# Optimization experiments

Measured on AMD Instinct MI355X. Metric: run time of the kernel, lower is better.

Reference implementation:

```python
import jax, jax.numpy as jnp
import numpy as np
from jax import lax

THRESH = 0.1  # stand-in for os.environ['THRESHOLD']
DN = ('NCHW', 'OIHW', 'NCHW')


def _prelu(x, a):
    # nn.PReLU() with a single shared parameter a (init 0.25)
    return jnp.where(x >= 0, x, a[0] * x)


def _nan_conv(x, w, b):
    # NaNConv2d: skip (zero out) input activations with |x| < THRESH,
    # then a standard 3x3 conv, stride 1, padding 1.
    xm = jnp.where(jnp.abs(x) >= THRESH, x, jnp.zeros((), x.dtype))
    y = lax.conv_general_dilated(xm, w, window_strides=(1, 1),
                                 padding='SAME', dimension_numbers=DN)
    return y + b[None, :, None, None]


def setup_inputs() -> dict:
    key = jax.random.key(0)
    ks = jax.random.split(key, 8)
    B, C, H, W = 8, 256, 128, 128
    x = jax.random.normal(ks[0], (B, C, H, W), dtype=jnp.float32)
    w_scale = 0.05  # keep activations numerically tame
    w1 = jax.random.normal(ks[1], (C, C, 3, 3), dtype=jnp.float32) * w_scale
    b1 = jax.random.normal(ks[2], (C,), dtype=jnp.float32) * w_scale
    w2 = jax.random.normal(ks[3], (C, C, 3, 3), dtype=jnp.float32) * w_scale
    b2 = jax.random.normal(ks[4], (C,), dtype=jnp.float32) * w_scale
    w3 = jax.random.normal(ks[5], (C, C, 3, 3), dtype=jnp.float32) * w_scale
    b3 = jax.random.normal(ks[6], (C,), dtype=jnp.float32) * w_scale
    prelu_a = jnp.full((1,), 0.25, dtype=jnp.float32)  # nn.PReLU default init
    return {'x': x, 'w1': w1, 'b1': b1, 'w2': w2, 'b2': b2,
            'w3': w3, 'b3': b3, 'prelu_a': prelu_a}


def reference(x, w1, b1, w2, b2, w3, b3, prelu_a):
    # x0 = NaNConv(prelu(x))
    x0 = _nan_conv(_prelu(x, prelu_a), w1, b1)
    # cat+max over trailing dim == elementwise max
    x1_max = jnp.maximum(x, x0)
    x1 = _prelu(x1_max, prelu_a)
    x1c = _nan_conv(x1, w2, b2)
    x2_max = jnp.maximum(x1c, x1_max)
    x2 = _prelu(x2_max, prelu_a)
    out = _nan_conv(x2, w3, b3)
    return out
```

## Files before the change

kernel.cpp:

```cpp
#include <hip/hip_runtime.h>
#include <cstddef>

#define THRESH 0.1f

constexpr int Bn = 8, C = 256, H = 128, W = 128;
constexpr int HW = H * W;
constexpr size_t CHW = (size_t)C * HW;
constexpr int WSZ = 9 * 256 * 256;

typedef __attribute__((ext_vector_type(8))) short short8;
typedef __attribute__((ext_vector_type(4))) float f32x4;

__device__ __forceinline__ float bf2f(ushort u) {
    union { unsigned u; float f; } v; v.u = ((unsigned)u) << 16; return v.f;
}
__device__ __forceinline__ ushort f2bf(float f) {
    union { float f; unsigned u; } v; v.f = f;
    unsigned r = v.u + 0x7FFF + ((v.u >> 16) & 1);
    return (ushort)(r >> 16);
}
__device__ __forceinline__ float pm(float x, float a) {
    float t = (x >= 0.f) ? x : a * x;
    return (fabsf(t) >= THRESH) ? t : 0.f;
}

__device__ __forceinline__ void load_lds16(const void* g, void* l) {
    __builtin_amdgcn_global_load_lds(
        (const __attribute__((address_space(1))) unsigned int*)g,
        (__attribute__((address_space(3))) unsigned int*)l, 16, 0, 0);
}

__global__ void wtrans_kernel(const float* __restrict__ w1,
                              const float* __restrict__ w2,
                              const float* __restrict__ w3,
                              ushort* __restrict__ Wtf)
{
    const float* src = (blockIdx.z == 0) ? w1 : (blockIdx.z == 1) ? w2 : w3;
    ushort* dst = Wtf + (size_t)blockIdx.z * WSZ;
    int idx = blockIdx.x * 256 + threadIdx.x;
    int co = idx >> 8, ci = idx & 255;
    int cb  = co >> 6;
    int m   = (co >> 4) & 3;
    int l15 = co & 15;
    int cib = ci >> 5;
    int l4  = (ci >> 3) & 3;
    int j   = ci & 7;
    int lane = l15 + 16 * l4;
    for (int t = 0; t < 9; ++t) {
        float v = src[((size_t)co * 256 + ci) * 9 + t];
        size_t o = ((((size_t)cb * 8 + cib) * 9 + t) * 4 + m) * 512 + lane * 8 + j;
        dst[o] = f2bf(v);
    }
}

__global__ __launch_bounds__(256) void xt1_kernel(const float* __restrict__ x,
                                                  const float* __restrict__ pa,
                                                  ushort* __restrict__ Xt)
{
    __shared__ float sl[64][133];
    int tid = threadIdx.x;
    int ci0 = blockIdx.x * 64, h = blockIdx.y, b = blockIdx.z;
    float a = pa[0];
    int wcol = tid & 127, chalf = tid >> 7;
    const float* xb = x + (size_t)b * CHW + (size_t)ci0 * HW + h * W;
    for (int r = 0; r < 32; ++r) {
        int ci = r * 2 + chalf;
        sl[ci][wcol] = pm(xb[(size_t)ci * HW + wcol], a);
    }
    __syncthreads();
    ushort* dst = Xt + ((size_t)(b * H + h)) * W * C + ci0;
    for (int r = 0; r < 4; ++r) {
        int c = r * 256 + tid;
        int wc = c >> 3, cic = c & 7;
        unsigned p0 = f2bf(sl[cic*8+0][wc]) | ((unsigned)f2bf(sl[cic*8+1][wc]) << 16);
        unsigned p1 = f2bf(sl[cic*8+2][wc]) | ((unsigned)f2bf(sl[cic*8+3][wc]) << 16);
        unsigned p2 = f2bf(sl[cic*8+4][wc]) | ((unsigned)f2bf(sl[cic*8+5][wc]) << 16);
        unsigned p3 = f2bf(sl[cic*8+6][wc]) | ((unsigned)f2bf(sl[cic*8+7][wc]) << 16);
        uint4 v = {p0, p1, p2, p3};
        *(uint4*)(dst + (size_t)wc * C + cic * 8) = v;
    }
}

template <int MODE>
__global__ __launch_bounds__(256, 2) void conv_kernel(
    const ushort* __restrict__ Xt, const ushort* __restrict__ Wtf,
    const float* __restrict__ bias, const float* __restrict__ pa,
    const float* __restrict__ xf,
    ushort* __restrict__ xmax,
    ushort* __restrict__ XtOut,
    float* __restrict__ out)
{
    __shared__ __align__(16) ushort sa[4 * 132 * 32];

    const int tid = threadIdx.x, lane = tid & 63, wv = tid >> 6;
    const int orig = blockIdx.x;
    const int vid = (orig & 7) * 256 + (orig >> 3);
    const int cb = vid & 3, by = vid >> 2;
    const int co0 = cb * 64;
    const int b = by >> 6, h0 = (by & 63) * 2;
    const int l15 = lane & 15, l4 = lane >> 4;
    const int hrow = wv >> 1, whalf = wv & 1;

    {
        uint4 z = {0, 0, 0, 0};
        uint4* zp = (uint4*)sa;
        for (int i = tid; i < 2112; i += 256) zp[i] = z;
    }

    f32x4 acc[4][4];
    const f32x4 z4 = {0.f, 0.f, 0.f, 0.f};
#pragma unroll
    for (int m = 0; m < 4; ++m)
#pragma unroll
        for (int n = 0; n < 4; ++n) acc[m][n] = z4;

    const ushort* xb = Xt + (size_t)b * H * W * C;
    const int sr = wv;
    const int shh = h0 - 1 + sr;
    const bool svalid = (unsigned)shh < 128u;
    const ushort* sgbase = xb + (size_t)shh * W * C;
    ushort* slbase = sa + (sr * 132 + 1) * 32;
    const int lchunk = lane >> 2, lsub = lane & 3;

    for (int cib = 0; cib < 8; ++cib) {
        const int ci0 = cib * 32;
        __syncthreads();
        if (svalid) {
#pragma unroll
            for (int seg = 0; seg < 8; ++seg) {
                int ww = seg * 16 + lchunk;
                int key = ((sr * 132 + 1 + ww) >> 1) & 3;
                const void* gp = sgbase + (size_t)ww * C + ci0 + ((lsub ^ key) << 3);
                load_lds16(gp, slbase + seg * 512);
            }
        }
        __syncthreads();

        const ushort* wB = Wtf + ((size_t)cb * 8 + cib) * 18432;
#pragma unroll
        for (int ky = 0; ky < 3; ++ky) {
            const int r = hrow + ky;
#pragma unroll
            for (int kx = 0; kx < 3; ++kx) {
                const int t = ky * 3 + kx;
                short8 af[4], bfv[4];
#pragma unroll
                for (int m = 0; m < 4; ++m)
                    af[m] = *(const short8*)(wB + (size_t)(t * 4 + m) * 512 + lane * 8);
#pragma unroll
                for (int n = 0; n < 4; ++n) {
                    int wi = whalf * 64 + n * 16 + l15 + kx;
                    int row = r * 132 + wi;
                    int key = (row >> 1) & 3;
                    bfv[n] = *(const short8*)(sa + row * 32 + ((l4 ^ key) << 3));
                }
#pragma unroll
                for (int m = 0; m < 4; ++m)
#pragma unroll
                    for (int n = 0; n < 4; ++n)
                        acc[m][n] = __builtin_amdgcn_mfma_f32_16x16x32_bf16(
                            af[m], bfv[n], acc[m][n], 0, 0, 0);
            }
        }
    }

    const int h = h0 + hrow;
    const float ap = (MODE != 0) ? pa[0] : 0.f;
#pragma unroll
    for (int m = 0; m < 4; ++m) {
        const int cobase = co0 + m * 16 + l4 * 4;
        const f32x4 bv = *(const f32x4*)(bias + cobase);
#pragma unroll
        for (int n = 0; n < 4; ++n) {
            const int wc = whalf * 64 + n * 16 + l15;
            if constexpr (MODE == 0) {
#pragma unroll
                for (int rr = 0; rr < 4; ++rr)
                    out[((size_t)(b * C + cobase + rr) * H + h) * W + wc] =
                        acc[m][n][rr] + bv[rr];
            } else {
                const size_t nb = ((size_t)(b * H + h) * W + wc) * C + cobase;
                float mm[4];
                if constexpr (MODE == 1) {
#pragma unroll
                    for (int rr = 0; rr < 4; ++rr) {
                        float vv = acc[m][n][rr] + bv[rr];
                        float xv = xf[((size_t)(b * C + cobase + rr) * H + h) * W + wc];
                        mm[rr] = fmaxf(xv, vv);
                    }
                    uint2 um = {(unsigned)f2bf(mm[0]) | ((unsigned)f2bf(mm[1]) << 16),
                                (unsigned)f2bf(mm[2]) | ((unsigned)f2bf(mm[3]) << 16)};
                    *(uint2*)(xmax + nb) = um;
                } else {
                    uint2 mv = *(const uint2*)(xmax + nb);
                    mm[0] = fmaxf(acc[m][n][0] + bv[0], bf2f((ushort)(mv.x & 0xffffu)));
                    mm[1] = fmaxf(acc[m][n][1] + bv[1], bf2f((ushort)(mv.x >> 16)));
                    mm[2] = fmaxf(acc[m][n][2] + bv[2], bf2f((ushort)(mv.y & 0xffffu)));
                    mm[3] = fmaxf(acc[m][n][3] + bv[3], bf2f((ushort)(mv.y >> 16)));
                }
                uint2 px = {(unsigned)f2bf(pm(mm[0], ap)) | ((unsigned)f2bf(pm(mm[1], ap)) << 16),
                            (unsigned)f2bf(pm(mm[2], ap)) | ((unsigned)f2bf(pm(mm[3], ap)) << 16)};
                *(uint2*)(XtOut + nb) = px;
            }
        }
    }
}

extern "C" void kernel_launch(void* const* d_in, const int* in_sizes, int n_in,
                              void* d_out, int out_size, void* d_ws, size_t ws_size,
                              hipStream_t stream)
{
    const float* x  = (const float*)d_in[0];
    const float* w1 = (const float*)d_in[1];
    const float* b1 = (const float*)d_in[2];
    const float* w2 = (const float*)d_in[3];
    const float* b2 = (const float*)d_in[4];
    const float* w3 = (const float*)d_in[5];
    const float* b3 = (const float*)d_in[6];
    const float* pa = (const float*)d_in[7];

    char* ws = (char*)d_ws;
    ushort* Xt1  = (ushort*)ws;
    ushort* Xt2  = (ushort*)(ws + 67108864);
    ushort* xmax = (ushort*)(ws + 134217728);
    ushort* Wtf  = (ushort*)(ws + 201326592);

    dim3 tg(4, 128, 8), tb(256);

    wtrans_kernel<<<dim3(256, 1, 3), 256, 0, stream>>>(w1, w2, w3, Wtf);
    xt1_kernel<<<tg, tb, 0, stream>>>(x, pa, Xt1);
    conv_kernel<1><<<dim3(2048), tb, 0, stream>>>(Xt1, Wtf, b1, pa, x, xmax, Xt2, nullptr);
    conv_kernel<2><<<dim3(2048), tb, 0, stream>>>(Xt2, Wtf + WSZ, b2, pa, nullptr, xmax, Xt1, nullptr);
    conv_kernel<0><<<dim3(2048), tb, 0, stream>>>(Xt1, Wtf + 2 * WSZ, b3, pa, nullptr, nullptr, nullptr, (float*)d_out);
}
```

Measured before the change: 766.1 us.

## Double-buffer LDS input tiles to overlap global loads with MFMA compute

Doubles the shared-memory input tile and switches it to dynamic LDS. The next channel block's global-to-LDS loads are issued before computing on the current buffer, which hides load latency behind the MFMA work. This leaves one barrier per iteration instead of two. LDS per block doubles to about 67 KB, which may limit how many blocks fit per CU alongside the launch bound of 2.

```diff
diff --git a/kernel.cpp b/kernel.cpp
--- a/kernel.cpp
+++ b/kernel.cpp
@@ -7,6 +7,8 @@
 constexpr int HW = H * W;
 constexpr size_t CHW = (size_t)C * HW;
 constexpr int WSZ = 9 * 256 * 256;
+constexpr int SA_ELEM = 4 * 132 * 32;
+constexpr int SA_BYTES = 2 * SA_ELEM * 2;
 
 typedef __attribute__((ext_vector_type(8))) short short8;
 typedef __attribute__((ext_vector_type(4))) float f32x4;
@@ -90,7 +92,7 @@
     ushort* __restrict__ XtOut,
     float* __restrict__ out)
 {
-    __shared__ __align__(16) ushort sa[4 * 132 * 32];
+    extern __shared__ __align__(16) ushort sa[];
 
     const int tid = threadIdx.x, lane = tid & 63, wv = tid >> 6;
     const int orig = blockIdx.x;
@@ -104,8 +106,9 @@
     {
         uint4 z = {0, 0, 0, 0};
         uint4* zp = (uint4*)sa;
-        for (int i = tid; i < 2112; i += 256) zp[i] = z;
-    }
+        for (int i = tid; i < 4224; i += 256) zp[i] = z;
+    }
+    __syncthreads();
 
     f32x4 acc[4][4];
     const f32x4 z4 = {0.f, 0.f, 0.f, 0.f};
@@ -119,23 +122,29 @@
     const int shh = h0 - 1 + sr;
     const bool svalid = (unsigned)shh < 128u;
     const ushort* sgbase = xb + (size_t)shh * W * C;
-    ushort* slbase = sa + (sr * 132 + 1) * 32;
     const int lchunk = lane >> 2, lsub = lane & 3;
 
+    auto stage = [&](int buf, int ci0) {
+        ushort* slb = sa + buf * SA_ELEM + (sr * 132 + 1) * 32;
+#pragma unroll
+        for (int seg = 0; seg < 8; ++seg) {
+            int ww = seg * 16 + lchunk;
+            int key = ((sr * 132 + 1 + ww) >> 1) & 3;
+            const void* gp = sgbase + (size_t)ww * C + ci0 + ((lsub ^ key) << 3);
+            load_lds16(gp, slb + seg * 512);
+        }
+    };
+
+    if (svalid) stage(0, 0);
+    asm volatile("s_waitcnt vmcnt(0)" ::: "memory");
+    __builtin_amdgcn_s_barrier();
+    __builtin_amdgcn_sched_barrier(0);
+
     for (int cib = 0; cib < 8; ++cib) {
-        const int ci0 = cib * 32;
-        __syncthreads();
-        if (svalid) {
-#pragma unroll
-            for (int seg = 0; seg < 8; ++seg) {
-                int ww = seg * 16 + lchunk;
-                int key = ((sr * 132 + 1 + ww) >> 1) & 3;
-                const void* gp = sgbase + (size_t)ww * C + ci0 + ((lsub ^ key) << 3);
-                load_lds16(gp, slbase + seg * 512);
-            }
-        }
-        __syncthreads();
-
+        const int cur = cib & 1;
+        if (cib < 7 && svalid) stage(cur ^ 1, (cib + 1) * 32);
+
+        const ushort* scur = sa + cur * SA_ELEM;
         const ushort* wB = Wtf + ((size_t)cb * 8 + cib) * 18432;
 #pragma unroll
         for (int ky = 0; ky < 3; ++ky) {
@@ -152,7 +161,7 @@
                     int wi = whalf * 64 + n * 16 + l15 + kx;
                     int row = r * 132 + wi;
                     int key = (row >> 1) & 3;
-                    bfv[n] = *(const short8*)(sa + row * 32 + ((l4 ^ key) << 3));
+                    bfv[n] = *(const short8*)(scur + row * 32 + ((l4 ^ key) << 3));
                 }
 #pragma unroll
                 for (int m = 0; m < 4; ++m)
@@ -162,6 +171,9 @@
                             af[m], bfv[n], acc[m][n], 0, 0, 0);
             }
         }
+        asm volatile("s_waitcnt vmcnt(0)" ::: "memory");
+        __builtin_amdgcn_s_barrier();
+        __builtin_amdgcn_sched_barrier(0);
     }
 
     const int h = h0 + hrow;
@@ -225,11 +237,22 @@
     ushort* xmax = (ushort*)(ws + 134217728);
     ushort* Wtf  = (ushort*)(ws + 201326592);
 
+    static bool attr_done = false;
+    if (!attr_done) {
+        hipFuncSetAttribute((const void*)conv_kernel<0>,
+                            hipFuncAttributeMaxDynamicSharedMemorySize, SA_BYTES);
+        hipFuncSetAttribute((const void*)conv_kernel<1>,
+                            hipFuncAttributeMaxDynamicSharedMemorySize, SA_BYTES);
+        hipFuncSetAttribute((const void*)conv_kernel<2>,
+                            hipFuncAttributeMaxDynamicSharedMemorySize, SA_BYTES);
+        attr_done = true;
+    }
+
     dim3 tg(4, 128, 8), tb(256);
 
     wtrans_kernel<<<dim3(256, 1, 3), 256, 0, stream>>>(w1, w2, w3, Wtf);
     xt1_kernel<<<tg, tb, 0, stream>>>(x, pa, Xt1);
-    conv_kernel<1><<<dim3(2048), tb, 0, stream>>>(Xt1, Wtf, b1, pa, x, xmax, Xt2, nullptr);
-    conv_kernel<2><<<dim3(2048), tb, 0, stream>>>(Xt2, Wtf + WSZ, b2, pa, nullptr, xmax, Xt1, nullptr);
-    conv_kernel<0><<<dim3(2048), tb, 0, stream>>>(Xt1, Wtf + 2 * WSZ, b3, pa, nullptr, nullptr, nullptr, (float*)d_out);
-}
+    conv_kernel<1><<<dim3(2048), tb, SA_BYTES, stream>>>(Xt1, Wtf, b1, pa, x, xmax, Xt2, nullptr);
+    conv_kernel<2><<<dim3(2048), tb, SA_BYTES, stream>>>(Xt2, Wtf + WSZ, b2, pa, nullptr, xmax, Xt1, nullptr);
+    conv_kernel<0><<<dim3(2048), tb, SA_BYTES, stream>>>(Xt1, Wtf + 2 * WSZ, b3, pa, nullptr, nullptr, nullptr, (float*)d_out);
+}
```

Result: slower. 1.297 ms (+69.4%).
